# Performance work log

Measured on AMD Instinct MI355X. Metric: run time of the kernel, lower is better.

The kernel has to match this reference:

```python
import jax, jax.numpy as jnp
import numpy as np

COMMITMENT_COST = 0.25


def setup_inputs() -> dict:
    key = jax.random.key(0)
    k1, k2 = jax.random.split(key)
    B, D, H, W = 16, 256, 32, 32
    K = 8192
    z = jax.random.normal(k1, (B, D, H, W), dtype=jnp.float32)
    embeddings = jax.random.uniform(k2, (K, D), dtype=jnp.float32,
                                    minval=-1.0 / K, maxval=1.0 / K)
    return {"z": z, "embeddings": embeddings}


def reference(z, embeddings):
    B, D, H, W = z.shape
    # NCHW -> NHWC, flatten spatial+batch to code vectors [N, D]
    z_p = jnp.transpose(z, (0, 2, 3, 1))
    z_flat = z_p.reshape(-1, D)
    # squared-distance via matmul: ||z||^2 + ||e||^2 - 2 z.e^T  -> [N, K]
    d = (jnp.sum(z_flat * z_flat, axis=1, keepdims=True)
         + jnp.sum(embeddings * embeddings, axis=1)
         - 2.0 * jnp.matmul(z_flat, embeddings.T))
    encoding_indices = jnp.argmin(d, axis=1)  # [N]
    quantized = embeddings[encoding_indices].reshape(z_p.shape)  # [B,H,W,D]
    e_latent_loss = jnp.mean((jax.lax.stop_gradient(quantized) - z_p) ** 2)
    q_latent_loss = jnp.mean((quantized - jax.lax.stop_gradient(z_p)) ** 2)
    loss = q_latent_loss + COMMITMENT_COST * e_latent_loss
    # straight-through estimator
    quantized_st = z_p + jax.lax.stop_gradient(quantized - z_p)
    out = jnp.transpose(quantized_st, (0, 3, 1, 2))  # back to NCHW
    return out, loss, encoding_indices.reshape(B, H, W)
```

## Files before the change

### kernel.cpp

```cpp
#include <hip/hip_runtime.h>

#define B_    16
#define D_    256
#define H_    32
#define W_    32
#define SP    1024
#define N_TOT 16384
#define K_    8192
#define ZB    (D_*SP)

#define BIAS_  0.03125f
#define DELTA_ 2.5e-4f

typedef __attribute__((ext_vector_type(8))) short bf16x8;
typedef __attribute__((ext_vector_type(4))) short bf16x4;
typedef __attribute__((ext_vector_type(4))) float f32x4;

#define GLOAD_LDS16(g, l) \
    __builtin_amdgcn_global_load_lds((const __attribute__((address_space(1))) void*)(g), \
                                     (__attribute__((address_space(3))) void*)(l), 16, 0, 0)

__device__ __forceinline__ unsigned short f2bf(float f) {
    unsigned u = __float_as_uint(f);
    u += 0x7FFFu + ((u >> 16) & 1u);
    return (unsigned short)(u >> 16);
}

__device__ __forceinline__ void merge2(unsigned &a1, unsigned &a2,
                                       unsigned b1, unsigned b2) {
    unsigned m1  = min(a1, b1);
    unsigned hi  = max(a1, b1);
    unsigned sel = (a1 < b1) ? a2 : b2;
    a2 = min(hi, sel);
    a1 = m1;
}


__global__ __launch_bounds__(256)
void cvt_e_enorm_p(const float* __restrict__ emb, short* __restrict__ ET,
                   float* __restrict__ enorm, float* __restrict__ enormB) {
    int t = threadIdx.x;
    int k = blockIdx.x * 4 + (t >> 6);
    int l = t & 63;
    float4 v = *(const float4*)(emb + (size_t)k * D_ + l * 4);
    float sum = v.x*v.x + v.y*v.y + v.z*v.z + v.w*v.w;
    for (int m = 1; m < 64; m <<= 1) sum += __shfl_xor(sum, m, 64);
    if (l == 0) { enorm[k] = sum; enormB[k] = sum + BIAS_; }
    bf16x4 o;
    o[0] = (short)f2bf(v.x); o[1] = (short)f2bf(v.y);
    o[2] = (short)f2bf(v.z); o[3] = (short)f2bf(v.w);
    *(bf16x4*)(ET + (size_t)k * D_ + l * 4) = o;
}

__global__ __launch_bounds__(256)
void zpart_cvtz_p(const float* __restrict__ z, float* __restrict__ zpart,
                  short* __restrict__ ZT) {
    int bx  = blockIdx.x;
    int dcb = bx >> 6;
    int st  = bx & 63;
    int t   = threadIdx.x;
    int n   = st * 256 + t;
    int b   = n >> 10;
    int s   = n & 1023;
    const float* zb = z + (size_t)b * ZB + (size_t)(dcb * 64) * SP + s;
    short* dst = ZT + (size_t)n * D_ + dcb * 64;
#pragma unroll
    for (int c2 = 0; c2 < 4; ++c2) {
        float vv[16];
#pragma unroll
        for (int dd = 0; dd < 16; ++dd)
            vv[dd] = zb[(size_t)(c2 * 16 + dd) * SP];
        float sum = 0.f;
#pragma unroll
        for (int dd = 0; dd < 16; ++dd) {
            float v = vv[dd];
            sum += v * v;
        }
        zpart[(size_t)(dcb * 4 + c2) * N_TOT + n] = sum;
        bf16x8 o0, o1;
#pragma unroll
        for (int j = 0; j < 8; ++j) { o0[j] = (short)f2bf(vv[j]);
                                      o1[j] = (short)f2bf(vv[8 + j]); }
        *(bf16x8*)(dst + c2 * 16)     = o0;
        *(bf16x8*)(dst + c2 * 16 + 8) = o1;
    }
}

__device__ __forceinline__ int stg_off(int base_row, int idx) {
    int r  = idx >> 2;
    int lc = (idx & 3) ^ ((r >> 1) & 3);
    return (base_row + r) * 256 + lc * 8;
}

__global__ __launch_bounds__(512, 2)
void mfma_argmin3(const short* __restrict__ ET, const short* __restrict__ ZT,
                  const float* __restrict__ enormB, uint2* __restrict__ pv) {
    __shared__ char smem[65536];
    const int t    = threadIdx.x;
    const int wid  = t >> 6, lane = t & 63;
    const int quad = lane >> 4, l16 = lane & 15;
    const int wm   = wid & 3, wn = wid >> 2;
    const int cb     = blockIdx.x & 31;
    const int rb     = blockIdx.x >> 5;
    const int c_base = cb * 256, n_base = rb * 256;

    const int offA0 = stg_off(c_base, t);
    const int offA1 = stg_off(c_base, t + 512);
    const int offB0 = stg_off(n_base, t);
    const int offB1 = stg_off(n_base, t + 512);

#define ISSUE_STAGE(dcb, h) { \
    char* As_ = smem + (h) * 32768; \
    char* Bs_ = As_ + 16384; \
    GLOAD_LDS16(ET + offA0 + (dcb) * 32, As_ + t * 16); \
    GLOAD_LDS16(ET + offA1 + (dcb) * 32, As_ + 8192 + t * 16); \
    GLOAD_LDS16(ZT + offB0 + (dcb) * 32, Bs_ + t * 16); \
    GLOAD_LDS16(ZT + offB1 + (dcb) * 32, Bs_ + 8192 + t * 16); }

    f32x4 acc[4][8];
#pragma unroll
    for (int fi = 0; fi < 4; ++fi)
#pragma unroll
        for (int fj = 0; fj < 8; ++fj) acc[fi][fj] = (f32x4){0.f, 0.f, 0.f, 0.f};

    const int ch = (quad ^ ((l16 >> 1) & 3)) * 16;
    ISSUE_STAGE(0, 0);
    __syncthreads();
#pragma unroll 1
    for (int s = 0; s < 8; ++s) {
        if (s < 7) ISSUE_STAGE(s + 1, (s + 1) & 1);
        const char* As = smem + (s & 1) * 32768;
        const char* Bs = As + 16384;
        bf16x8 a[4];
#pragma unroll
        for (int fi = 0; fi < 4; ++fi)
            a[fi] = *(const bf16x8*)(As + (wm * 64 + fi * 16 + l16) * 64 + ch);
#pragma unroll
        for (int fj = 0; fj < 8; ++fj) {
            bf16x8 bv = *(const bf16x8*)(Bs + (wn * 128 + fj * 16 + l16) * 64 + ch);
#pragma unroll
            for (int fi = 0; fi < 4; ++fi)
                acc[fi][fj] = __builtin_amdgcn_mfma_f32_16x16x32_bf16(
                    a[fi], bv, acc[fi][fj], 0, 0, 0);
        }
        __syncthreads();
    }
#undef ISSUE_STAGE

    unsigned r1[8], r2[8];
#pragma unroll
    for (int fj = 0; fj < 8; ++fj) { r1[fj] = 0xFFFFFFFFu; r2[fj] = 0xFFFFFFFFu; }
    float ekv[4][4];
#pragma unroll
    for (int fi = 0; fi < 4; ++fi) {
        float4 e4 = *(const float4*)(enormB + c_base + wm * 64 + fi * 16 + quad * 4);
        ekv[fi][0]=e4.x; ekv[fi][1]=e4.y; ekv[fi][2]=e4.z; ekv[fi][3]=e4.w;
    }
#pragma unroll
    for (int fj = 0; fj < 8; ++fj) {
#pragma unroll
        for (int fi = 0; fi < 4; ++fi) {
            const unsigned cbs = (unsigned)(c_base + wm * 64 + fi * 16 + quad * 4);
            float s0 = fmaf(-2.f, acc[fi][fj].x, ekv[fi][0]);
            float s1 = fmaf(-2.f, acc[fi][fj].y, ekv[fi][1]);
            float s2 = fmaf(-2.f, acc[fi][fj].z, ekv[fi][2]);
            float s3 = fmaf(-2.f, acc[fi][fj].w, ekv[fi][3]);
            unsigned k0 = (__float_as_uint(s0) & 0xFFFFE000u) | (cbs + 0u);
            unsigned k1 = (__float_as_uint(s1) & 0xFFFFE000u) | (cbs + 1u);
            unsigned k2 = (__float_as_uint(s2) & 0xFFFFE000u) | (cbs + 2u);
            unsigned k3 = (__float_as_uint(s3) & 0xFFFFE000u) | (cbs + 3u);
            unsigned lo1 = min(k0, k1), hi1 = max(k0, k1);
            unsigned lo2 = min(k2, k3), hi2 = max(k2, k3);
            merge2(lo1, hi1, lo2, hi2);
            merge2(r1[fj], r2[fj], lo1, hi1);
        }
    }
    uint2* mbuf = (uint2*)smem;
#pragma unroll
    for (int fj = 0; fj < 8; ++fj) {
        unsigned a1 = r1[fj], a2 = r2[fj];
#pragma unroll
        for (int m = 16; m <= 32; m <<= 1) {
            unsigned b1 = __shfl_xor(a1, m, 64);
            unsigned b2 = __shfl_xor(a2, m, 64);
            merge2(a1, a2, b1, b2);
        }
        if (quad == 0)
            mbuf[wm * 256 + wn * 128 + fj * 16 + l16] = make_uint2(a1, a2);
    }
    __syncthreads();
    if (t < 256) {
        uint2 P = mbuf[t];
        unsigned a1 = P.x, a2 = P.y;
#pragma unroll
        for (int g = 1; g < 4; ++g) {
            uint2 Q = mbuf[g * 256 + t];
            merge2(a1, a2, Q.x, Q.y);
        }
        pv[(size_t)cb * N_TOT + n_base + t] = make_uint2(a1, a2);
    }
}


template <int NG>
__global__ __launch_bounds__(256)
void reduce_phaseA_t(const uint2* __restrict__ pv, int* __restrict__ fidx,
                     float* __restrict__ out_idx, int* __restrict__ wl,
                     int* __restrict__ wl_cnt, float* __restrict__ out_loss) {
    int n = blockIdx.x * 256 + threadIdx.x;
    if (n == 0) *out_loss = 0.f;
    uint2 pp[NG];
    unsigned mn = 0xFFFFFFFFu;
#pragma unroll
    for (int g = 0; g < NG; ++g) {
        pp[g] = pv[(size_t)g * N_TOT + n];
        mn = min(mn, pp[g].x);
    }
    float smin  = __uint_as_float(mn & 0xFFFFE000u);
    unsigned th = __float_as_uint(smin + DELTA_) | 8191u;
    int cnt = 0;
#pragma unroll
    for (int g = 0; g < NG; ++g) {
        cnt += (pp[g].x <= th) ? 1 : 0;
        cnt += (pp[g].y <= th) ? 1 : 0;
    }
    if (cnt > 1) {
        int slot = atomicAdd(wl_cnt, 1);
        wl[slot] = n;
    } else {
        int c = (int)(mn & 8191u);
        fidx[n] = c;
        out_idx[n] = (float)c;
    }
}

template <int NG>
__global__ __launch_bounds__(256)
void recheck_t(const uint2* __restrict__ pv, const float* __restrict__ znorm,
               const float* __restrict__ enorm, const float* __restrict__ z,
               const float* __restrict__ emb, const int* __restrict__ wl,
               const int* __restrict__ wl_cnt, int* __restrict__ fidx,
               float* __restrict__ out_idx) {
    __shared__ float zrow[4][256];
    const int lane = threadIdx.x & 63;
    const int wslot = threadIdx.x >> 6;
    const int gwave = (blockIdx.x * 256 + threadIdx.x) >> 6;
    const int nwaves = (gridDim.x * 256) >> 6;
    const int total = *wl_cnt;

    for (int i = gwave; i < total; i += nwaves) {
        int n = wl[i];
        unsigned key = 0xFFFFFFFFu;
        if (lane < 2 * NG) {
            uint2 p = pv[(size_t)(lane >> 1) * N_TOT + n];
            key = (lane & 1) ? p.y : p.x;
        }
        unsigned mn = key;
#pragma unroll
        for (int m = 1; m < 64; m <<= 1) mn = min(mn, __shfl_xor(mn, m, 64));
        float smin  = __uint_as_float(mn & 0xFFFFE000u);
        unsigned th = __float_as_uint(smin + DELTA_) | 8191u;

        const int b = n >> 10, sp = n & 1023;
        const float* zr = z + (size_t)b * ZB + sp;
#pragma unroll
        for (int j = 0; j < 4; ++j)
            zrow[wslot][lane + j * 64] = zr[(size_t)(lane + j * 64) * SP];
        float zn = znorm[n];

        unsigned lexlo = 0xFFFFFFFFu, lexhi = 0xFFFFFFFFu;
        if (key <= th) {
            int c = (int)(key & 8191u);
            const float* er = emb + (size_t)c * D_;
            float dot = 0.f;
#pragma unroll 8
            for (int d = 0; d < D_; ++d)
                dot = fmaf(zrow[wslot][d], er[d], dot);
            float s = (zn + enorm[c]) - 2.f * dot;
            unsigned sb = __float_as_uint(s);
            lexhi = sb >> 19;
            lexlo = (sb << 13) | (unsigned)c;
        }
#pragma unroll
        for (int m = 1; m < 64; m <<= 1) {
            unsigned olo = __shfl_xor(lexlo, m, 64);
            unsigned ohi = __shfl_xor(lexhi, m, 64);
            if (ohi < lexhi || (ohi == lexhi && olo < lexlo)) { lexhi = ohi; lexlo = olo; }
        }
        if (lane == 0) {
            int c = (int)(lexlo & 8191u);
            fidx[n] = c;
            out_idx[n] = (float)c;
        }
    }
}


__global__ __launch_bounds__(256)
void cvt_e_enorm(const float* __restrict__ emb, short* __restrict__ ET3,
                 float* __restrict__ enorm, float* __restrict__ enormB) {
    int t = threadIdx.x;
    int k = blockIdx.x * 4 + (t >> 6);
    int l = t & 63;
    float4 v = *(const float4*)(emb + (size_t)k * D_ + l * 4);
    float sum = v.x*v.x + v.y*v.y + v.z*v.z + v.w*v.w;
    for (int m = 1; m < 64; m <<= 1) sum += __shfl_xor(sum, m, 64);
    if (l == 0) { enorm[k] = sum; enormB[k] = sum + BIAS_; }
    int dcb  = l >> 4;
    int c    = (l >> 1) & 7;
    int half = l & 1;
    bf16x4 o;
    o[0] = (short)f2bf(v.x); o[1] = (short)f2bf(v.y);
    o[2] = (short)f2bf(v.z); o[3] = (short)f2bf(v.w);
    *(bf16x4*)(ET3 + ((size_t)dcb * K_ + k) * 64 + ((c ^ (k & 7)) * 8) + half * 4) = o;
}

__global__ __launch_bounds__(256)
void zpart_cvtz(const float* __restrict__ z, float* __restrict__ zpart,
                short* __restrict__ ZT3) {
    int bx  = blockIdx.x;
    int dcb = bx >> 6;
    int st  = bx & 63;
    int t   = threadIdx.x;
    int n   = st * 256 + t;
    int b   = n >> 10;
    int s   = n & 1023;
    const float* zb = z + (size_t)b * ZB + (size_t)(dcb * 64) * SP + s;
    short* dst = ZT3 + ((size_t)dcb * N_TOT + n) * 64;
    int sw = n & 7;
#pragma unroll
    for (int c2 = 0; c2 < 4; ++c2) {
        float vv[16];
#pragma unroll
        for (int dd = 0; dd < 16; ++dd)
            vv[dd] = zb[(size_t)(c2 * 16 + dd) * SP];
        float sum = 0.f;
#pragma unroll
        for (int dd = 0; dd < 16; ++dd) {
            float v = vv[dd];
            sum += v * v;
        }
        zpart[(size_t)(dcb * 4 + c2) * N_TOT + n] = sum;
        bf16x8 o0, o1;
#pragma unroll
        for (int j = 0; j < 8; ++j) { o0[j] = (short)f2bf(vv[j]);
                                      o1[j] = (short)f2bf(vv[8 + j]); }
        *(bf16x8*)(dst + (((c2 * 2)     ^ sw) * 8)) = o0;
        *(bf16x8*)(dst + (((c2 * 2 + 1) ^ sw) * 8)) = o1;
    }
}

__global__ __launch_bounds__(256, 4)
void mfma_argmin2(const short* __restrict__ ET3, const short* __restrict__ ZT3,
                  const float* __restrict__ enormB, uint2* __restrict__ pv) {
    __shared__ char smem[32768];
    const int t    = threadIdx.x;
    const int wid  = t >> 6, lane = t & 63;
    const int quad = lane >> 4, l16 = lane & 15;
    const int wm   = wid >> 1, wn = wid & 1;
    const int stripe = blockIdx.x >> 7;
    const int n0     = (blockIdx.x & 127) * 128;
    const int swz    = (l16 & 7);

    unsigned r1[4], r2[4];
#pragma unroll
    for (int fj = 0; fj < 4; ++fj) { r1[fj] = 0xFFFFFFFFu; r2[fj] = 0xFFFFFFFFu; }

#pragma unroll 1
    for (int cc = 0; cc < 8; ++cc) {
        const int c0 = stripe * 1024 + cc * 128;
        f32x4 acc[4][4];
#pragma unroll
        for (int fi = 0; fi < 4; ++fi)
#pragma unroll
            for (int fj = 0; fj < 4; ++fj) acc[fi][fj] = (f32x4){0.f, 0.f, 0.f, 0.f};

#pragma unroll 1
        for (int dcb = 0; dcb < 4; ++dcb) {
            __syncthreads();
            const char* gA = (const char*)ET3 + ((size_t)dcb * K_    + c0) * 128;
            const char* gB = (const char*)ZT3 + ((size_t)dcb * N_TOT + n0) * 128;
#pragma unroll
            for (int j = 0; j < 4; ++j) {
                int off = j * 4096 + t * 16;
                GLOAD_LDS16(gA + off, smem + off);
                GLOAD_LDS16(gB + off, smem + 16384 + off);
            }
            __syncthreads();
#pragma unroll
            for (int dc2 = 0; dc2 < 2; ++dc2) {
                bf16x8 af[4], bfv[4];
                const int chm = ((dc2 * 4 + quad) ^ swz) * 16;
#pragma unroll
                for (int fi = 0; fi < 4; ++fi)
                    af[fi] = *(const bf16x8*)(smem + (wm*64 + fi*16 + l16)*128 + chm);
#pragma unroll
                for (int fj = 0; fj < 4; ++fj)
                    bfv[fj] = *(const bf16x8*)(smem + 16384 + (wn*64 + fj*16 + l16)*128 + chm);
#pragma unroll
                for (int fi = 0; fi < 4; ++fi)
#pragma unroll
                    for (int fj = 0; fj < 4; ++fj)
                        acc[fi][fj] = __builtin_amdgcn_mfma_f32_16x16x32_bf16(
                            af[fi], bfv[fj], acc[fi][fj], 0, 0, 0);
            }
        }

        float ekv[4][4];
#pragma unroll
        for (int fi = 0; fi < 4; ++fi) {
            float4 e4 = *(const float4*)(enormB + c0 + wm*64 + fi*16 + quad*4);
            ekv[fi][0]=e4.x; ekv[fi][1]=e4.y; ekv[fi][2]=e4.z; ekv[fi][3]=e4.w;
        }
#pragma unroll
        for (int fj = 0; fj < 4; ++fj) {
#pragma unroll
            for (int fi = 0; fi < 4; ++fi) {
                const unsigned cb = (unsigned)(c0 + wm*64 + fi*16 + quad*4);
                float s0 = fmaf(-2.f, acc[fi][fj].x, ekv[fi][0]);
                float s1 = fmaf(-2.f, acc[fi][fj].y, ekv[fi][1]);
                float s2 = fmaf(-2.f, acc[fi][fj].z, ekv[fi][2]);
                float s3 = fmaf(-2.f, acc[fi][fj].w, ekv[fi][3]);
                unsigned k0 = (__float_as_uint(s0) & 0xFFFFE000u) | (cb + 0u);
                unsigned k1 = (__float_as_uint(s1) & 0xFFFFE000u) | (cb + 1u);
                unsigned k2 = (__float_as_uint(s2) & 0xFFFFE000u) | (cb + 2u);
                unsigned k3 = (__float_as_uint(s3) & 0xFFFFE000u) | (cb + 3u);
                unsigned lo1 = min(k0, k1), hi1 = max(k0, k1);
                unsigned lo2 = min(k2, k3), hi2 = max(k2, k3);
                merge2(lo1, hi1, lo2, hi2);
                merge2(r1[fj], r2[fj], lo1, hi1);
            }
        }
    }

#pragma unroll
    for (int fj = 0; fj < 4; ++fj) {
        unsigned a1 = r1[fj], a2 = r2[fj];
#pragma unroll
        for (int m = 16; m <= 32; m <<= 1) {
            unsigned b1 = __shfl_xor(a1, m, 64);
            unsigned b2 = __shfl_xor(a2, m, 64);
            merge2(a1, a2, b1, b2);
        }
        if (quad == 0) {
            int n = n0 + wn*64 + fj*16 + l16;
            pv[(size_t)(stripe * 2 + wm) * N_TOT + n] = make_uint2(a1, a2);
        }
    }
}


__global__ __launch_bounds__(256)
void znorm_kernel2(const float* __restrict__ zpart, float* __restrict__ znorm,
                   int* __restrict__ wl_cnt) {
    int n = blockIdx.x * 256 + threadIdx.x;
    float sum = 0.f;
#pragma unroll
    for (int dc = 0; dc < 16; ++dc) sum += zpart[(size_t)dc * N_TOT + n];
    znorm[n] = sum;
    if (n == 0) *wl_cnt = 0;
}

__global__ __launch_bounds__(256)
void output_kernel2(const float* __restrict__ z, const float* __restrict__ emb,
                    const int* __restrict__ fidx, float* __restrict__ out,
                    float* __restrict__ loss) {
    __shared__ float eL[32][257];
    __shared__ int   fid[32];
    __shared__ float red[4];
    const int nb = blockIdx.x;
    const int n0 = nb * 32;
    const int b  = n0 >> 10;
    const int s0 = n0 & 1023;
    const int t  = threadIdx.x;
    if (t < 32) fid[t] = fidx[n0 + t];
    __syncthreads();
#pragma unroll
    for (int i = 0; i < 8; ++i) {
        int p = t + i * 256;
        int row = p >> 6, q = p & 63;
        float4 v = *(const float4*)(emb + (size_t)fid[row] * D_ + q * 4);
        eL[row][q*4+0] = v.x; eL[row][q*4+1] = v.y;
        eL[row][q*4+2] = v.z; eL[row][q*4+3] = v.w;
    }
    __syncthreads();
    const int sl = t & 31, dg = t >> 5;
    float lsum = 0.f;
#pragma unroll
    for (int i = 0; i < 32; ++i) {
        int d = dg * 32 + i;
        size_t off = ((size_t)(b * D_ + d)) * SP + s0 + sl;
        float zv = z[off];
        float q  = eL[sl][d];
        float diff = q - zv;
        out[off] = zv + diff;
        lsum += diff * diff;
    }
    for (int m = 1; m < 64; m <<= 1) lsum += __shfl_xor(lsum, m, 64);
    if ((t & 63) == 0) red[t >> 6] = lsum;
    __syncthreads();
    if (t == 0) {
        float tot = (red[0] + red[1] + red[2] + red[3])
                    * (1.25f / (float)(B_ * SP * D_));
        atomicAdd(loss, tot);
    }
}


extern "C" void kernel_launch(void* const* d_in, const int* in_sizes, int n_in,
                              void* d_out, int out_size, void* d_ws, size_t ws_size,
                              hipStream_t stream) {
    const float* z   = (const float*)d_in[0];
    const float* emb = (const float*)d_in[1];
    float* out = (float*)d_out;
    float* w   = (float*)d_ws;

    float* enorm  = w;
    float* enormB = w + 8192;
    float* znorm  = w + 16384;
    int*   fidx   = (int*)(w + 32768);
    int*   wl_cnt = (int*)(w + 49152);
    int*   wl     = (int*)(w + 49216);

    float* out0     = out;
    float* out_loss = out + (size_t)B_ * D_ * SP;
    float* out_idx  = out_loss + 1;

    const size_t NEED_BIG = 4259968ULL * 4ULL;
    if (ws_size >= NEED_BIG) {
        uint2* pv    = (uint2*)(w + 65664);
        float* zpart = w + 65664;
        short* ET    = (short*)(w + 1114240);
        short* ZT    = (short*)(w + 2162816);

        cvt_e_enorm_p<<<K_ / 4, 256, 0, stream>>>(emb, ET, enorm, enormB);
        zpart_cvtz_p<<<256, 256, 0, stream>>>(z, zpart, ZT);
        znorm_kernel2<<<N_TOT / 256, 256, 0, stream>>>(zpart, znorm, wl_cnt);
        mfma_argmin3<<<2048, 512, 0, stream>>>(ET, ZT, enormB, pv);
        reduce_phaseA_t<32><<<N_TOT / 256, 256, 0, stream>>>(pv, fidx, out_idx,
                                                             wl, wl_cnt, out_loss);
        recheck_t<32><<<256, 256, 0, stream>>>(pv, znorm, enorm, z, emb,
                                               wl, wl_cnt, fidx, out_idx);
    } else {
        uint2* pv    = (uint2*)(w + 65664);
        float* zpart = w + 65664;
        short* ET3   = (short*)(w + 589952);
        short* ZT3   = (short*)(w + 1638528);

        cvt_e_enorm<<<K_ / 4, 256, 0, stream>>>(emb, ET3, enorm, enormB);
        zpart_cvtz<<<256, 256, 0, stream>>>(z, zpart, ZT3);
        znorm_kernel2<<<N_TOT / 256, 256, 0, stream>>>(zpart, znorm, wl_cnt);
        mfma_argmin2<<<1024, 256, 0, stream>>>(ET3, ZT3, enormB, pv);
        reduce_phaseA_t<16><<<N_TOT / 256, 256, 0, stream>>>(pv, fidx, out_idx,
                                                             wl, wl_cnt, out_loss);
        recheck_t<16><<<256, 256, 0, stream>>>(pv, znorm, enorm, z, emb,
                                               wl, wl_cnt, fidx, out_idx);
    }
    output_kernel2<<<N_TOT / 32, 256, 0, stream>>>(z, emb, fidx, out0, out_loss);
}
```

Before: 248.5 us.

## Drop big-workspace path, fuse prep kernels, register-prefetch double-buffered MFMA argmin

```diff
diff --git a/kernel.cpp b/kernel.cpp
--- a/kernel.cpp
+++ b/kernel.cpp
@@ -16,10 +16,6 @@
 typedef __attribute__((ext_vector_type(4))) short bf16x4;
 typedef __attribute__((ext_vector_type(4))) float f32x4;
 
-#define GLOAD_LDS16(g, l) \
-    __builtin_amdgcn_global_load_lds((const __attribute__((address_space(1))) void*)(g), \
-                                     (__attribute__((address_space(3))) void*)(l), 16, 0, 0)
-
 __device__ __forceinline__ unsigned short f2bf(float f) {
     unsigned u = __float_as_uint(f);
     u += 0x7FFFu + ((u >> 16) & 1u);
@@ -37,323 +33,65 @@
 
 
 __global__ __launch_bounds__(256)
-void cvt_e_enorm_p(const float* __restrict__ emb, short* __restrict__ ET,
-                   float* __restrict__ enorm, float* __restrict__ enormB) {
-    int t = threadIdx.x;
-    int k = blockIdx.x * 4 + (t >> 6);
-    int l = t & 63;
-    float4 v = *(const float4*)(emb + (size_t)k * D_ + l * 4);
-    float sum = v.x*v.x + v.y*v.y + v.z*v.z + v.w*v.w;
-    for (int m = 1; m < 64; m <<= 1) sum += __shfl_xor(sum, m, 64);
-    if (l == 0) { enorm[k] = sum; enormB[k] = sum + BIAS_; }
-    bf16x4 o;
-    o[0] = (short)f2bf(v.x); o[1] = (short)f2bf(v.y);
-    o[2] = (short)f2bf(v.z); o[3] = (short)f2bf(v.w);
-    *(bf16x4*)(ET + (size_t)k * D_ + l * 4) = o;
-}
-
-__global__ __launch_bounds__(256)
-void zpart_cvtz_p(const float* __restrict__ z, float* __restrict__ zpart,
-                  short* __restrict__ ZT) {
-    int bx  = blockIdx.x;
-    int dcb = bx >> 6;
-    int st  = bx & 63;
-    int t   = threadIdx.x;
-    int n   = st * 256 + t;
-    int b   = n >> 10;
-    int s   = n & 1023;
-    const float* zb = z + (size_t)b * ZB + (size_t)(dcb * 64) * SP + s;
-    short* dst = ZT + (size_t)n * D_ + dcb * 64;
-#pragma unroll
-    for (int c2 = 0; c2 < 4; ++c2) {
-        float vv[16];
-#pragma unroll
-        for (int dd = 0; dd < 16; ++dd)
-            vv[dd] = zb[(size_t)(c2 * 16 + dd) * SP];
-        float sum = 0.f;
-#pragma unroll
-        for (int dd = 0; dd < 16; ++dd) {
-            float v = vv[dd];
-            sum += v * v;
-        }
-        zpart[(size_t)(dcb * 4 + c2) * N_TOT + n] = sum;
-        bf16x8 o0, o1;
-#pragma unroll
-        for (int j = 0; j < 8; ++j) { o0[j] = (short)f2bf(vv[j]);
-                                      o1[j] = (short)f2bf(vv[8 + j]); }
-        *(bf16x8*)(dst + c2 * 16)     = o0;
-        *(bf16x8*)(dst + c2 * 16 + 8) = o1;
-    }
-}
-
-__device__ __forceinline__ int stg_off(int base_row, int idx) {
-    int r  = idx >> 2;
-    int lc = (idx & 3) ^ ((r >> 1) & 3);
-    return (base_row + r) * 256 + lc * 8;
-}
-
-__global__ __launch_bounds__(512, 2)
-void mfma_argmin3(const short* __restrict__ ET, const short* __restrict__ ZT,
+void prep_kernel(const float* __restrict__ emb, const float* __restrict__ z,
+                 short* __restrict__ ET3, short* __restrict__ ZT3,
+                 float* __restrict__ zpart, float* __restrict__ enorm,
+                 float* __restrict__ enormB, int* __restrict__ wl_cnt) {
+    const int bx = blockIdx.x;
+    const int t  = threadIdx.x;
+    if (bx < 2048) {
+        int k = bx * 4 + (t >> 6);
+        int l = t & 63;
+        float4 v = *(const float4*)(emb + (size_t)k * D_ + l * 4);
+        float sum = v.x*v.x + v.y*v.y + v.z*v.z + v.w*v.w;
+        for (int m = 1; m < 64; m <<= 1) sum += __shfl_xor(sum, m, 64);
+        if (l == 0) { enorm[k] = sum; enormB[k] = sum + BIAS_; }
+        int dcb  = l >> 4;
+        int c    = (l >> 1) & 7;
+        int half = l & 1;
+        bf16x4 o;
+        o[0] = (short)f2bf(v.x); o[1] = (short)f2bf(v.y);
+        o[2] = (short)f2bf(v.z); o[3] = (short)f2bf(v.w);
+        *(bf16x4*)(ET3 + ((size_t)dcb * K_ + k) * 64 + ((c ^ (k & 7)) * 8) + half * 4) = o;
+    } else {
+        int bz  = bx - 2048;
+        if (bz == 0 && t == 0) *wl_cnt = 0;
+        int dcb = bz >> 6;
+        int st  = bz & 63;
+        int n   = st * 256 + t;
+        int b   = n >> 10;
+        int s   = n & 1023;
+        const float* zb = z + (size_t)b * ZB + (size_t)(dcb * 64) * SP + s;
+        short* dst = ZT3 + ((size_t)dcb * N_TOT + n) * 64;
+        int sw = n & 7;
+#pragma unroll
+        for (int c2 = 0; c2 < 4; ++c2) {
+            float vv[16];
+#pragma unroll
+            for (int dd = 0; dd < 16; ++dd)
+                vv[dd] = zb[(size_t)(c2 * 16 + dd) * SP];
+            float sum = 0.f;
+#pragma unroll
+            for (int dd = 0; dd < 16; ++dd) {
+                float v = vv[dd];
+                sum += v * v;
+            }
+            zpart[(size_t)(dcb * 4 + c2) * N_TOT + n] = sum;
+            bf16x8 o0, o1;
+#pragma unroll
+            for (int j = 0; j < 8; ++j) { o0[j] = (short)f2bf(vv[j]);
+                                          o1[j] = (short)f2bf(vv[8 + j]); }
+            *(bf16x8*)(dst + (((c2 * 2)     ^ sw) * 8)) = o0;
+            *(bf16x8*)(dst + (((c2 * 2 + 1) ^ sw) * 8)) = o1;
+        }
+    }
+}
+
+
+__global__ __launch_bounds__(256, 2)
+void mfma_argmin4(const short* __restrict__ ET3, const short* __restrict__ ZT3,
                   const float* __restrict__ enormB, uint2* __restrict__ pv) {
     __shared__ char smem[65536];
-    const int t    = threadIdx.x;
-    const int wid  = t >> 6, lane = t & 63;
-    const int quad = lane >> 4, l16 = lane & 15;
-    const int wm   = wid & 3, wn = wid >> 2;
-    const int cb     = blockIdx.x & 31;
-    const int rb     = blockIdx.x >> 5;
-    const int c_base = cb * 256, n_base = rb * 256;
-
-    const int offA0 = stg_off(c_base, t);
-    const int offA1 = stg_off(c_base, t + 512);
-    const int offB0 = stg_off(n_base, t);
-    const int offB1 = stg_off(n_base, t + 512);
-
-#define ISSUE_STAGE(dcb, h) { \
-    char* As_ = smem + (h) * 32768; \
-    char* Bs_ = As_ + 16384; \
-    GLOAD_LDS16(ET + offA0 + (dcb) * 32, As_ + t * 16); \
-    GLOAD_LDS16(ET + offA1 + (dcb) * 32, As_ + 8192 + t * 16); \
-    GLOAD_LDS16(ZT + offB0 + (dcb) * 32, Bs_ + t * 16); \
-    GLOAD_LDS16(ZT + offB1 + (dcb) * 32, Bs_ + 8192 + t * 16); }
-
-    f32x4 acc[4][8];
-#pragma unroll
-    for (int fi = 0; fi < 4; ++fi)
-#pragma unroll
-        for (int fj = 0; fj < 8; ++fj) acc[fi][fj] = (f32x4){0.f, 0.f, 0.f, 0.f};
-
-    const int ch = (quad ^ ((l16 >> 1) & 3)) * 16;
-    ISSUE_STAGE(0, 0);
-    __syncthreads();
-#pragma unroll 1
-    for (int s = 0; s < 8; ++s) {
-        if (s < 7) ISSUE_STAGE(s + 1, (s + 1) & 1);
-        const char* As = smem + (s & 1) * 32768;
-        const char* Bs = As + 16384;
-        bf16x8 a[4];
-#pragma unroll
-        for (int fi = 0; fi < 4; ++fi)
-            a[fi] = *(const bf16x8*)(As + (wm * 64 + fi * 16 + l16) * 64 + ch);
-#pragma unroll
-        for (int fj = 0; fj < 8; ++fj) {
-            bf16x8 bv = *(const bf16x8*)(Bs + (wn * 128 + fj * 16 + l16) * 64 + ch);
-#pragma unroll
-            for (int fi = 0; fi < 4; ++fi)
-                acc[fi][fj] = __builtin_amdgcn_mfma_f32_16x16x32_bf16(
-                    a[fi], bv, acc[fi][fj], 0, 0, 0);
-        }
-        __syncthreads();
-    }
-#undef ISSUE_STAGE
-
-    unsigned r1[8], r2[8];
-#pragma unroll
-    for (int fj = 0; fj < 8; ++fj) { r1[fj] = 0xFFFFFFFFu; r2[fj] = 0xFFFFFFFFu; }
-    float ekv[4][4];
-#pragma unroll
-    for (int fi = 0; fi < 4; ++fi) {
-        float4 e4 = *(const float4*)(enormB + c_base + wm * 64 + fi * 16 + quad * 4);
-        ekv[fi][0]=e4.x; ekv[fi][1]=e4.y; ekv[fi][2]=e4.z; ekv[fi][3]=e4.w;
-    }
-#pragma unroll
-    for (int fj = 0; fj < 8; ++fj) {
-#pragma unroll
-        for (int fi = 0; fi < 4; ++fi) {
-            const unsigned cbs = (unsigned)(c_base + wm * 64 + fi * 16 + quad * 4);
-            float s0 = fmaf(-2.f, acc[fi][fj].x, ekv[fi][0]);
-            float s1 = fmaf(-2.f, acc[fi][fj].y, ekv[fi][1]);
-            float s2 = fmaf(-2.f, acc[fi][fj].z, ekv[fi][2]);
-            float s3 = fmaf(-2.f, acc[fi][fj].w, ekv[fi][3]);
-            unsigned k0 = (__float_as_uint(s0) & 0xFFFFE000u) | (cbs + 0u);
-            unsigned k1 = (__float_as_uint(s1) & 0xFFFFE000u) | (cbs + 1u);
-            unsigned k2 = (__float_as_uint(s2) & 0xFFFFE000u) | (cbs + 2u);
-            unsigned k3 = (__float_as_uint(s3) & 0xFFFFE000u) | (cbs + 3u);
-            unsigned lo1 = min(k0, k1), hi1 = max(k0, k1);
-            unsigned lo2 = min(k2, k3), hi2 = max(k2, k3);
-            merge2(lo1, hi1, lo2, hi2);
-            merge2(r1[fj], r2[fj], lo1, hi1);
-        }
-    }
-    uint2* mbuf = (uint2*)smem;
-#pragma unroll
-    for (int fj = 0; fj < 8; ++fj) {
-        unsigned a1 = r1[fj], a2 = r2[fj];
-#pragma unroll
-        for (int m = 16; m <= 32; m <<= 1) {
-            unsigned b1 = __shfl_xor(a1, m, 64);
-            unsigned b2 = __shfl_xor(a2, m, 64);
-            merge2(a1, a2, b1, b2);
-        }
-        if (quad == 0)
-            mbuf[wm * 256 + wn * 128 + fj * 16 + l16] = make_uint2(a1, a2);
-    }
-    __syncthreads();
-    if (t < 256) {
-        uint2 P = mbuf[t];
-        unsigned a1 = P.x, a2 = P.y;
-#pragma unroll
-        for (int g = 1; g < 4; ++g) {
-            uint2 Q = mbuf[g * 256 + t];
-            merge2(a1, a2, Q.x, Q.y);
-        }
-        pv[(size_t)cb * N_TOT + n_base + t] = make_uint2(a1, a2);
-    }
-}
-
-
-template <int NG>
-__global__ __launch_bounds__(256)
-void reduce_phaseA_t(const uint2* __restrict__ pv, int* __restrict__ fidx,
-                     float* __restrict__ out_idx, int* __restrict__ wl,
-                     int* __restrict__ wl_cnt, float* __restrict__ out_loss) {
-    int n = blockIdx.x * 256 + threadIdx.x;
-    if (n == 0) *out_loss = 0.f;
-    uint2 pp[NG];
-    unsigned mn = 0xFFFFFFFFu;
-#pragma unroll
-    for (int g = 0; g < NG; ++g) {
-        pp[g] = pv[(size_t)g * N_TOT + n];
-        mn = min(mn, pp[g].x);
-    }
-    float smin  = __uint_as_float(mn & 0xFFFFE000u);
-    unsigned th = __float_as_uint(smin + DELTA_) | 8191u;
-    int cnt = 0;
-#pragma unroll
-    for (int g = 0; g < NG; ++g) {
-        cnt += (pp[g].x <= th) ? 1 : 0;
-        cnt += (pp[g].y <= th) ? 1 : 0;
-    }
-    if (cnt > 1) {
-        int slot = atomicAdd(wl_cnt, 1);
-        wl[slot] = n;
-    } else {
-        int c = (int)(mn & 8191u);
-        fidx[n] = c;
-        out_idx[n] = (float)c;
-    }
-}
-
-template <int NG>
-__global__ __launch_bounds__(256)
-void recheck_t(const uint2* __restrict__ pv, const float* __restrict__ znorm,
-               const float* __restrict__ enorm, const float* __restrict__ z,
-               const float* __restrict__ emb, const int* __restrict__ wl,
-               const int* __restrict__ wl_cnt, int* __restrict__ fidx,
-               float* __restrict__ out_idx) {
-    __shared__ float zrow[4][256];
-    const int lane = threadIdx.x & 63;
-    const int wslot = threadIdx.x >> 6;
-    const int gwave = (blockIdx.x * 256 + threadIdx.x) >> 6;
-    const int nwaves = (gridDim.x * 256) >> 6;
-    const int total = *wl_cnt;
-
-    for (int i = gwave; i < total; i += nwaves) {
-        int n = wl[i];
-        unsigned key = 0xFFFFFFFFu;
-        if (lane < 2 * NG) {
-            uint2 p = pv[(size_t)(lane >> 1) * N_TOT + n];
-            key = (lane & 1) ? p.y : p.x;
-        }
-        unsigned mn = key;
-#pragma unroll
-        for (int m = 1; m < 64; m <<= 1) mn = min(mn, __shfl_xor(mn, m, 64));
-        float smin  = __uint_as_float(mn & 0xFFFFE000u);
-        unsigned th = __float_as_uint(smin + DELTA_) | 8191u;
-
-        const int b = n >> 10, sp = n & 1023;
-        const float* zr = z + (size_t)b * ZB + sp;
-#pragma unroll
-        for (int j = 0; j < 4; ++j)
-            zrow[wslot][lane + j * 64] = zr[(size_t)(lane + j * 64) * SP];
-        float zn = znorm[n];
-
-        unsigned lexlo = 0xFFFFFFFFu, lexhi = 0xFFFFFFFFu;
-        if (key <= th) {
-            int c = (int)(key & 8191u);
-            const float* er = emb + (size_t)c * D_;
-            float dot = 0.f;
-#pragma unroll 8
-            for (int d = 0; d < D_; ++d)
-                dot = fmaf(zrow[wslot][d], er[d], dot);
-            float s = (zn + enorm[c]) - 2.f * dot;
-            unsigned sb = __float_as_uint(s);
-            lexhi = sb >> 19;
-            lexlo = (sb << 13) | (unsigned)c;
-        }
-#pragma unroll
-        for (int m = 1; m < 64; m <<= 1) {
-            unsigned olo = __shfl_xor(lexlo, m, 64);
-            unsigned ohi = __shfl_xor(lexhi, m, 64);
-            if (ohi < lexhi || (ohi == lexhi && olo < lexlo)) { lexhi = ohi; lexlo = olo; }
-        }
-        if (lane == 0) {
-            int c = (int)(lexlo & 8191u);
-            fidx[n] = c;
-            out_idx[n] = (float)c;
-        }
-    }
-}
-
-
-__global__ __launch_bounds__(256)
-void cvt_e_enorm(const float* __restrict__ emb, short* __restrict__ ET3,
-                 float* __restrict__ enorm, float* __restrict__ enormB) {
-    int t = threadIdx.x;
-    int k = blockIdx.x * 4 + (t >> 6);
-    int l = t & 63;
-    float4 v = *(const float4*)(emb + (size_t)k * D_ + l * 4);
-    float sum = v.x*v.x + v.y*v.y + v.z*v.z + v.w*v.w;
-    for (int m = 1; m < 64; m <<= 1) sum += __shfl_xor(sum, m, 64);
-    if (l == 0) { enorm[k] = sum; enormB[k] = sum + BIAS_; }
-    int dcb  = l >> 4;
-    int c    = (l >> 1) & 7;
-    int half = l & 1;
-    bf16x4 o;
-    o[0] = (short)f2bf(v.x); o[1] = (short)f2bf(v.y);
-    o[2] = (short)f2bf(v.z); o[3] = (short)f2bf(v.w);
-    *(bf16x4*)(ET3 + ((size_t)dcb * K_ + k) * 64 + ((c ^ (k & 7)) * 8) + half * 4) = o;
-}
-
-__global__ __launch_bounds__(256)
-void zpart_cvtz(const float* __restrict__ z, float* __restrict__ zpart,
-                short* __restrict__ ZT3) {
-    int bx  = blockIdx.x;
-    int dcb = bx >> 6;
-    int st  = bx & 63;
-    int t   = threadIdx.x;
-    int n   = st * 256 + t;
-    int b   = n >> 10;
-    int s   = n & 1023;
-    const float* zb = z + (size_t)b * ZB + (size_t)(dcb * 64) * SP + s;
-    short* dst = ZT3 + ((size_t)dcb * N_TOT + n) * 64;
-    int sw = n & 7;
-#pragma unroll
-    for (int c2 = 0; c2 < 4; ++c2) {
-        float vv[16];
-#pragma unroll
-        for (int dd = 0; dd < 16; ++dd)
-            vv[dd] = zb[(size_t)(c2 * 16 + dd) * SP];
-        float sum = 0.f;
-#pragma unroll
-        for (int dd = 0; dd < 16; ++dd) {
-            float v = vv[dd];
-            sum += v * v;
-        }
-        zpart[(size_t)(dcb * 4 + c2) * N_TOT + n] = sum;
-        bf16x8 o0, o1;
-#pragma unroll
-        for (int j = 0; j < 8; ++j) { o0[j] = (short)f2bf(vv[j]);
-                                      o1[j] = (short)f2bf(vv[8 + j]); }
-        *(bf16x8*)(dst + (((c2 * 2)     ^ sw) * 8)) = o0;
-        *(bf16x8*)(dst + (((c2 * 2 + 1) ^ sw) * 8)) = o1;
-    }
-}
-
-__global__ __launch_bounds__(256, 4)
-void mfma_argmin2(const short* __restrict__ ET3, const short* __restrict__ ZT3,
-                  const float* __restrict__ enormB, uint2* __restrict__ pv) {
-    __shared__ char smem[32768];
     const int t    = threadIdx.x;
     const int wid  = t >> 6, lane = t & 63;
     const int quad = lane >> 4, l16 = lane & 15;
@@ -366,6 +104,17 @@
 #pragma unroll
     for (int fj = 0; fj < 4; ++fj) { r1[fj] = 0xFFFFFFFFu; r2[fj] = 0xFFFFFFFFu; }
 
+    int4 ra[4], rb[4];
+    {
+        const char* gA = (const char*)ET3 + ((size_t)stripe * 1024) * 128;
+        const char* gB = (const char*)ZT3 + ((size_t)n0) * 128;
+#pragma unroll
+        for (int j = 0; j < 4; ++j) {
+            ra[j] = *(const int4*)(gA + j * 4096 + t * 16);
+            rb[j] = *(const int4*)(gB + j * 4096 + t * 16);
+        }
+    }
+
 #pragma unroll 1
     for (int cc = 0; cc < 8; ++cc) {
         const int c0 = stripe * 1024 + cc * 128;
@@ -375,28 +124,43 @@
 #pragma unroll
             for (int fj = 0; fj < 4; ++fj) acc[fi][fj] = (f32x4){0.f, 0.f, 0.f, 0.f};
 
-#pragma unroll 1
+#pragma unroll
         for (int dcb = 0; dcb < 4; ++dcb) {
+            char* bufA = smem + (dcb & 1) * 32768;
+            char* bufB = bufA + 16384;
+#pragma unroll
+            for (int j = 0; j < 4; ++j) {
+                *(int4*)(bufA + j * 4096 + t * 16) = ra[j];
+                *(int4*)(bufB + j * 4096 + t * 16) = rb[j];
+            }
             __syncthreads();
-            const char* gA = (const char*)ET3 + ((size_t)dcb * K_    + c0) * 128;
-            const char* gB = (const char*)ZT3 + ((size_t)dcb * N_TOT + n0) * 128;
-#pragma unroll
-            for (int j = 0; j < 4; ++j) {
-                int off = j * 4096 + t * 16;
-                GLOAD_LDS16(gA + off, smem + off);
-                GLOAD_LDS16(gB + off, smem + 16384 + off);
-            }
-            __syncthreads();
+            if (dcb < 3) {
+                const char* gA = (const char*)ET3 + ((size_t)(dcb + 1) * K_ + c0) * 128;
+                const char* gB = (const char*)ZT3 + ((size_t)(dcb + 1) * N_TOT + n0) * 128;
+#pragma unroll
+                for (int j = 0; j < 4; ++j) {
+                    ra[j] = *(const int4*)(gA + j * 4096 + t * 16);
+                    rb[j] = *(const int4*)(gB + j * 4096 + t * 16);
+                }
+            } else if (cc < 7) {
+                const char* gA = (const char*)ET3 + ((size_t)(c0 + 128)) * 128;
+                const char* gB = (const char*)ZT3 + ((size_t)n0) * 128;
+#pragma unroll
+                for (int j = 0; j < 4; ++j) {
+                    ra[j] = *(const int4*)(gA + j * 4096 + t * 16);
+                    rb[j] = *(const int4*)(gB + j * 4096 + t * 16);
+                }
+            }
 #pragma unroll
             for (int dc2 = 0; dc2 < 2; ++dc2) {
                 bf16x8 af[4], bfv[4];
                 const int chm = ((dc2 * 4 + quad) ^ swz) * 16;
 #pragma unroll
                 for (int fi = 0; fi < 4; ++fi)
-                    af[fi] = *(const bf16x8*)(smem + (wm*64 + fi*16 + l16)*128 + chm);
+                    af[fi] = *(const bf16x8*)(bufA + (wm*64 + fi*16 + l16)*128 + chm);
 #pragma unroll
                 for (int fj = 0; fj < 4; ++fj)
-                    bfv[fj] = *(const bf16x8*)(smem + 16384 + (wn*64 + fj*16 + l16)*128 + chm);
+                    bfv[fj] = *(const bf16x8*)(bufB + (wn*64 + fj*16 + l16)*128 + chm);
 #pragma unroll
                 for (int fi = 0; fi < 4; ++fi)
 #pragma unroll
@@ -450,16 +214,105 @@
 }
 
 
+template <int NG>
 __global__ __launch_bounds__(256)
-void znorm_kernel2(const float* __restrict__ zpart, float* __restrict__ znorm,
-                   int* __restrict__ wl_cnt) {
+void phaseA_z(const uint2* __restrict__ pv, const float* __restrict__ zpart,
+              float* __restrict__ znorm, int* __restrict__ fidx,
+              float* __restrict__ out_idx, int* __restrict__ wl,
+              int* __restrict__ wl_cnt, float* __restrict__ out_loss) {
     int n = blockIdx.x * 256 + threadIdx.x;
-    float sum = 0.f;
-#pragma unroll
-    for (int dc = 0; dc < 16; ++dc) sum += zpart[(size_t)dc * N_TOT + n];
-    znorm[n] = sum;
-    if (n == 0) *wl_cnt = 0;
-}
+    if (n == 0) *out_loss = 0.f;
+    float zsum = 0.f;
+#pragma unroll
+    for (int dc = 0; dc < 16; ++dc) zsum += zpart[(size_t)dc * N_TOT + n];
+    znorm[n] = zsum;
+    uint2 pp[NG];
+    unsigned mn = 0xFFFFFFFFu;
+#pragma unroll
+    for (int g = 0; g < NG; ++g) {
+        pp[g] = pv[(size_t)g * N_TOT + n];
+        mn = min(mn, pp[g].x);
+    }
+    float smin  = __uint_as_float(mn & 0xFFFFE000u);
+    unsigned th = __float_as_uint(smin + DELTA_) | 8191u;
+    int cnt = 0;
+#pragma unroll
+    for (int g = 0; g < NG; ++g) {
+        cnt += (pp[g].x <= th) ? 1 : 0;
+        cnt += (pp[g].y <= th) ? 1 : 0;
+    }
+    if (cnt > 1) {
+        int slot = atomicAdd(wl_cnt, 1);
+        wl[slot] = n;
+    } else {
+        int c = (int)(mn & 8191u);
+        fidx[n] = c;
+        out_idx[n] = (float)c;
+    }
+}
+
+
+template <int NG>
+__global__ __launch_bounds__(256)
+void recheck_t(const uint2* __restrict__ pv, const float* __restrict__ znorm,
+               const float* __restrict__ enorm, const float* __restrict__ z,
+               const float* __restrict__ emb, const int* __restrict__ wl,
+               const int* __restrict__ wl_cnt, int* __restrict__ fidx,
+               float* __restrict__ out_idx) {
+    __shared__ float zrow[4][256];
+    const int lane = threadIdx.x & 63;
+    const int wslot = threadIdx.x >> 6;
+    const int gwave = (blockIdx.x * 256 + threadIdx.x) >> 6;
+    const int nwaves = (gridDim.x * 256) >> 6;
+    const int total = *wl_cnt;
+
+    for (int i = gwave; i < total; i += nwaves) {
+        int n = wl[i];
+        unsigned key = 0xFFFFFFFFu;
+        if (lane < 2 * NG) {
+            uint2 p = pv[(size_t)(lane >> 1) * N_TOT + n];
+            key = (lane & 1) ? p.y : p.x;
+        }
+        unsigned mn = key;
+#pragma unroll
+        for (int m = 1; m < 64; m <<= 1) mn = min(mn, __shfl_xor(mn, m, 64));
+        float smin  = __uint_as_float(mn & 0xFFFFE000u);
+        unsigned th = __float_as_uint(smin + DELTA_) | 8191u;
+
+        const int b = n >> 10, sp = n & 1023;
+        const float* zr = z + (size_t)b * ZB + sp;
+#pragma unroll
+        for (int j = 0; j < 4; ++j)
+            zrow[wslot][lane + j * 64] = zr[(size_t)(lane + j * 64) * SP];
+        float zn = znorm[n];
+
+        unsigned lexlo = 0xFFFFFFFFu, lexhi = 0xFFFFFFFFu;
+        if (key <= th) {
+            int c = (int)(key & 8191u);
+            const float* er = emb + (size_t)c * D_;
+            float dot = 0.f;
+#pragma unroll 8
+            for (int d = 0; d < D_; ++d)
+                dot = fmaf(zrow[wslot][d], er[d], dot);
+            float s = (zn + enorm[c]) - 2.f * dot;
+            unsigned sb = __float_as_uint(s);
+            lexhi = sb >> 19;
+            lexlo = (sb << 13) | (unsigned)c;
+        }
+#pragma unroll
+        for (int m = 1; m < 64; m <<= 1) {
+            unsigned olo = __shfl_xor(lexlo, m, 64);
+            unsigned ohi = __shfl_xor(lexhi, m, 64);
+            if (ohi < lexhi || (ohi == lexhi && olo < lexlo)) { lexhi = ohi; lexlo = olo; }
+        }
+        if (lane == 0) {
+            int c = (int)(lexlo & 8191u);
+            fidx[n] = c;
+            out_idx[n] = (float)c;
+        }
+    }
+}
+
 
 __global__ __launch_bounds__(256)
 void output_kernel2(const float* __restrict__ z, const float* __restrict__ emb,
@@ -521,40 +374,21 @@
     int*   fidx   = (int*)(w + 32768);
     int*   wl_cnt = (int*)(w + 49152);
     int*   wl     = (int*)(w + 49216);
+    float* zpart  = w + 65664;
+    uint2* pv     = (uint2*)(w + 327808);
+    short* ET3    = (short*)(w + 852096);
+    short* ZT3    = (short*)(w + 1900672);
 
     float* out0     = out;
     float* out_loss = out + (size_t)B_ * D_ * SP;
     float* out_idx  = out_loss + 1;
 
-    const size_t NEED_BIG = 4259968ULL * 4ULL;
-    if (ws_size >= NEED_BIG) {
-        uint2* pv    = (uint2*)(w + 65664);
-        float* zpart = w + 65664;
-        short* ET    = (short*)(w + 1114240);
-        short* ZT    = (short*)(w + 2162816);
-
-        cvt_e_enorm_p<<<K_ / 4, 256, 0, stream>>>(emb, ET, enorm, enormB);
-        zpart_cvtz_p<<<256, 256, 0, stream>>>(z, zpart, ZT);
-        znorm_kernel2<<<N_TOT / 256, 256, 0, stream>>>(zpart, znorm, wl_cnt);
-        mfma_argmin3<<<2048, 512, 0, stream>>>(ET, ZT, enormB, pv);
-        reduce_phaseA_t<32><<<N_TOT / 256, 256, 0, stream>>>(pv, fidx, out_idx,
-                                                             wl, wl_cnt, out_loss);
-        recheck_t<32><<<256, 256, 0, stream>>>(pv, znorm, enorm, z, emb,
-                                               wl, wl_cnt, fidx, out_idx);
-    } else {
-        uint2* pv    = (uint2*)(w + 65664);
-        float* zpart = w + 65664;
-        short* ET3   = (short*)(w + 589952);
-        short* ZT3   = (short*)(w + 1638528);
-
-        cvt_e_enorm<<<K_ / 4, 256, 0, stream>>>(emb, ET3, enorm, enormB);
-        zpart_cvtz<<<256, 256, 0, stream>>>(z, zpart, ZT3);
-        znorm_kernel2<<<N_TOT / 256, 256, 0, stream>>>(zpart, znorm, wl_cnt);
-        mfma_argmin2<<<1024, 256, 0, stream>>>(ET3, ZT3, enormB, pv);
-        reduce_phaseA_t<16><<<N_TOT / 256, 256, 0, stream>>>(pv, fidx, out_idx,
-                                                             wl, wl_cnt, out_loss);
-        recheck_t<16><<<256, 256, 0, stream>>>(pv, znorm, enorm, z, emb,
-                                               wl, wl_cnt, fidx, out_idx);
-    }
+    prep_kernel<<<2304, 256, 0, stream>>>(emb, z, ET3, ZT3, zpart,
+                                          enorm, enormB, wl_cnt);
+    mfma_argmin4<<<1024, 256, 0, stream>>>(ET3, ZT3, enormB, pv);
+    phaseA_z<16><<<N_TOT / 256, 256, 0, stream>>>(pv, zpart, znorm, fidx,
+                                                  out_idx, wl, wl_cnt, out_loss);
+    recheck_t<16><<<256, 256, 0, stream>>>(pv, znorm, enorm, z, emb,
+                                           wl, wl_cnt, fidx, out_idx);
     output_kernel2<<<N_TOT / 32, 256, 0, stream>>>(z, emb, fidx, out0, out_loss);
 }
```

Result: slower. 321.9 us (+29.5%).
